# Kernel tuning notes

Measured on AMD Instinct MI355X. Metric: run time of the kernel, lower is better.

Reference implementation:

```python
import jax, jax.numpy as jnp
import numpy as np

KSIZE, SCALE, STRIDE, SOFTMAX_SCALE = 3, 3, 1, 10.0
ESCAPE_NAN = 1e-4
DN = ('NCHW', 'OIHW', 'NCHW')


def same_pad(x, k, stride):
    # torch same_padding: pad so out = ceil(in/stride)
    H, W = x.shape[-2], x.shape[-1]
    oh, ow = -(-H // stride), -(-W // stride)
    ph = max(0, (oh - 1) * stride + k - H)
    pw = max(0, (ow - 1) * stride + k - W)
    return jnp.pad(x, ((0, 0), (0, 0), (ph // 2, ph - ph // 2), (pw // 2, pw - pw // 2)))


def extract_patches(img, k, stride):
    # img [B,C,H,W] already padded -> [B, L, C, k, k], matching torch Unfold ordering (C slowest, kh, kw)
    B, C, H, W = img.shape
    oh, ow = (H - k) // stride + 1, (W - k) // stride + 1
    cols = [img[:, :, i:i + stride * oh:stride, j:j + stride * ow:stride]
            for i in range(k) for j in range(k)]
    p = jnp.stack(cols, axis=2)                      # [B, C, k*k, oh, ow]
    p = p.reshape(B, C, k, k, oh * ow)               # [B, C, k, k, L]
    return jnp.transpose(p, (0, 4, 1, 2, 3))         # [B, L, C, k, k]


def conv1x1_prelu(x, W, b, a):
    y = jnp.einsum('bchw,oc->bohw', x, W) + b[None, :, None, None]
    return jnp.where(y >= 0, y, a * y)


def bilinear_down(x, Ho, Wo):
    # F.interpolate(mode='bilinear', align_corners=False), no antialias
    H, W = x.shape[-2], x.shape[-1]
    def coords(o, s):
        src = (jnp.arange(o, dtype=jnp.float32) + 0.5) * (s / o) - 0.5
        src = jnp.clip(src, 0.0, s - 1.0)
        i0 = jnp.floor(src).astype(jnp.int32)
        i1 = jnp.minimum(i0 + 1, s - 1)
        return i0, i1, src - i0.astype(jnp.float32)
    y0, y1, wy = coords(Ho, H)
    x0, x1, wx = coords(Wo, W)
    r = x[:, :, y0, :] * (1.0 - wy)[:, None] + x[:, :, y1, :] * wy[:, None]
    return r[:, :, :, x0] * (1.0 - wx) + r[:, :, :, x1] * wx


def forward(x, Wa, ba, aa, Wm1, bm1, am1, Wm2, bm2, am2):
    B, C, H, W = x.shape
    kernel = SCALE * KSIZE  # 9
    embed_w = conv1x1_prelu(x, Wa, ba, aa)      # [B,C,H,W]
    match = conv1x1_prelu(x, Wm1, bm1, am1)     # [B,C/2,H,W]
    # large-scale patches used as conv_transpose kernels: [B, L, C, 9, 9]
    raw_w = extract_patches(same_pad(embed_w, kernel, STRIDE * SCALE), kernel, STRIDE * SCALE)
    Hr, Wr = H // SCALE, W // SCALE
    ref = conv1x1_prelu(bilinear_down(x, Hr, Wr), Wm2, bm2, am2)  # [B,C/2,Hr,Wr]
    # small-scale patches used as correlation kernels: [B, L, C/2, 3, 3]
    w = extract_patches(same_pad(ref, KSIZE, STRIDE), KSIZE, STRIDE)
    norm = jnp.sqrt(jnp.sum(w * w, axis=(2, 3, 4), keepdims=True))
    wn = w / jnp.maximum(norm, ESCAPE_NAN)
    xp = same_pad(match, KSIZE, 1)  # [B,C/2,H+2,W+2]

    def corr(xi, wi):  # xi [C/2,H+2,W+2], wi [L,C/2,3,3] -> [L,H,W]
        return jax.lax.conv_general_dilated(xi[None], wi, (1, 1), 'VALID', dimension_numbers=DN)[0]

    y = jax.vmap(corr)(xp, wn)                  # [B,L,H,W]
    y = jax.nn.softmax(y * SOFTMAX_SCALE, axis=1)

    pad = kernel - 1 - SCALE  # conv_transpose2d(stride=3, padding=3) equivalent padding = 5

    def tconv(yi, rwi):  # yi [L,H,W], rwi [L,C,9,9] -> [C,3H,3W]
        k = jnp.transpose(jnp.flip(rwi, (-2, -1)), (1, 0, 2, 3))  # [C,L,9,9]
        return jax.lax.conv_general_dilated(
            yi[None], k, (1, 1), [(pad, pad), (pad, pad)],
            lhs_dilation=(STRIDE * SCALE, STRIDE * SCALE), dimension_numbers=DN)[0]

    out = jax.vmap(tconv)(y, raw_w) / 6.0       # [B,C,3H,3W]
    return out


def setup_inputs() -> dict:
    key = jax.random.key(0)
    ks = jax.random.split(key, 8)
    B, C, H, W = 4, 64, 60, 60
    C2 = C // 2
    return {
        'x': jax.random.normal(ks[0], (B, C, H, W), jnp.float32),
        'Wa': jax.random.normal(ks[1], (C, C), jnp.float32) * 0.1,
        'ba': jax.random.normal(ks[2], (C,), jnp.float32) * 0.1,
        'aa': jnp.full((1,), 0.25, jnp.float32),
        'Wm1': jax.random.normal(ks[3], (C2, C), jnp.float32) * 0.1,
        'bm1': jax.random.normal(ks[4], (C2,), jnp.float32) * 0.1,
        'am1': jnp.full((1,), 0.25, jnp.float32),
        'Wm2': jax.random.normal(ks[5], (C2, C), jnp.float32) * 0.1,
        'bm2': jax.random.normal(ks[6], (C2,), jnp.float32) * 0.1,
        'am2': jnp.full((1,), 0.25, jnp.float32),
    }


def reference(x, Wa, ba, aa, Wm1, bm1, am1, Wm2, bm2, am2):
    return forward(x, Wa, ba, aa, Wm1, bm1, am1, Wm2, bm2, am2)
```

## Files before the change

### kernel.cpp

```cpp
#include <hip/hip_runtime.h>
#include <hip/hip_bf16.h>

typedef __hip_bfloat16 bf16_t;
using f32x4  = __attribute__((ext_vector_type(4))) float;
using bf16x8 = __attribute__((ext_vector_type(8))) short;

#define NB 4
#define NC 64
#define NC2 32
#define NH 60
#define NW 60
#define NPIX (NH*NW)
#define HP 66
#define MP 62
#define HR 20
#define RP 22
#define NL 400
#define OHW 180
#define KPAD 512

#define SZ_E   (NB*HP*HP*NC)
#define SZ_XP  (NB*NC2*MP*MP)
#define SZ_RP  (NB*NC2*RP*RP)
#define SZ_IN  (NB*NL)
#define SZ_Y   (NB*NPIX*NL)

__global__ __launch_bounds__(256) void k_conv(
    const float* __restrict__ x,
    const float* __restrict__ Wa,  const float* __restrict__ ba,  const float* __restrict__ aa,
    const float* __restrict__ Wm1, const float* __restrict__ bm1, const float* __restrict__ am1,
    const float* __restrict__ Wm2, const float* __restrict__ bm2, const float* __restrict__ am2,
    float* __restrict__ E_t, float* __restrict__ xp, float* __restrict__ refp) {
  int bid = blockIdx.x;
  int t = threadIdx.x;
  if (bid < 3600) {
    __shared__ float Ws[64*64];
    __shared__ float bs[64];
    __shared__ float al;
    int b = bid / 900, pblk = bid % 900;
    for (int i = t; i < 64*64; i += 256) {
      int co = i >> 6, c = i & 63;
      Ws[c*64 + co] = Wa[i];
    }
    if (t < 64) bs[t] = ba[t];
    if (t == 0) al = aa[0];
    __syncthreads();
    int lane = t & 63, wid = t >> 6;
    int pix = pblk*4 + wid;
    int ph = pix / NW, pw = pix % NW;
    const float* xb = x + b*NC*NPIX + pix;
    float acc = bs[lane];
    #pragma unroll 8
    for (int c = 0; c < 64; ++c)
      acc = fmaf(xb[c*NPIX], Ws[c*64 + lane], acc);
    acc = acc >= 0.f ? acc : al*acc;
    E_t[((b*HP + ph+3)*HP + (pw+3))*NC + lane] = acc;
  } else if (bid < 5400) {
    int idx = (bid - 3600)*256 + t;
    int pix = idx % NPIX; int tmp = idx / NPIX;
    int co = tmp % NC2; int b = tmp / NC2;
    float alpha = am1[0];
    const float* xb = x + b*NC*NPIX + pix;
    const float* wr = Wm1 + co*64;
    float acc = bm1[co];
    #pragma unroll 8
    for (int c = 0; c < 64; ++c)
      acc = fmaf(xb[c*NPIX], wr[c], acc);
    acc = acc >= 0.f ? acc : alpha*acc;
    int ph = pix / NW, pw = pix % NW;
    xp[((b*NC2 + co)*MP + ph+1)*MP + (pw+1)] = acc;
  } else {
    int idx = (bid - 5400)*256 + t;
    int pos = idx % (HR*HR); int tmp = idx / (HR*HR);
    int co = tmp % NC2; int b = tmp / NC2;
    int hr = pos / HR, wr_ = pos % HR;
    float alpha = am2[0];
    const float* xb = x + b*NC*NPIX + (3*hr+1)*NW + (3*wr_+1);
    const float* wrow = Wm2 + co*64;
    float acc = bm2[co];
    #pragma unroll 8
    for (int c = 0; c < 64; ++c)
      acc = fmaf(xb[c*NPIX], wrow[c], acc);
    acc = acc >= 0.f ? acc : alpha*acc;
    refp[((b*NC2 + co)*RP + hr+1)*RP + (wr_+1)] = acc;
  }
}

__global__ __launch_bounds__(64) void k_invn(
    const float* __restrict__ refp, float* __restrict__ invn) {
  int bl = blockIdx.x;
  int b = bl / NL, l = bl % NL;
  int lh = l / HR, lw = l % HR;
  int t = threadIdx.x;
  float ss = 0.f;
  for (int e = t; e < NC2*9; e += 64) {
    int c = e / 9, r = e % 9;
    int i = r / 3, j = r % 3;
    float v = refp[((b*NC2 + c)*RP + lh+i)*RP + (lw+j)];
    ss = fmaf(v, v, ss);
  }
  #pragma unroll
  for (int off = 32; off > 0; off >>= 1)
    ss += __shfl_xor(ss, off);
  if (t == 0) invn[bl] = 1.f / fmaxf(sqrtf(ss), 1e-4f);
}

__global__ __launch_bounds__(256) void k_swz(
    const float* __restrict__ xp, const float* __restrict__ refp,
    const float* __restrict__ invn, const float* __restrict__ E_t,
    bf16_t* __restrict__ Xp, bf16_t* __restrict__ Rf, bf16_t* __restrict__ Eb) {
  int bid = blockIdx.x;
  if (bid < 2025) {
    int tid = bid*256 + threadIdx.x;
    int slot = tid & 63; int rest = tid >> 6;
    int ks = rest % 9; int rest2 = rest / 9;
    int mblk = rest2 % 225; int b = rest2 / 225;
    int m = mblk*16 + (slot & 15);
    int h = m / NW, w = m % NW;
    int k0 = ks*32 + (slot >> 4)*8;
    const float* xb = xp + (size_t)b*NC2*MP*MP;
    union { bf16_t a[8]; bf16x8 v; } u;
    #pragma unroll
    for (int j = 0; j < 8; ++j) {
      int k = k0 + j;
      int c = k / 9, r = k % 9;
      int i = r / 3, j2 = r % 3;
      u.a[j] = __float2bfloat16(xb[(c*MP + h + i)*MP + w + j2]);
    }
    *(bf16x8*)(Xp + (size_t)tid*8) = u.v;
  } else if (bid < 2250) {
    int tid = (bid - 2025)*256 + threadIdx.x;
    int slot = tid & 63; int rest = tid >> 6;
    int ks = rest % 9; int rest2 = rest / 9;
    int nblk = rest2 % 25; int b = rest2 / 25;
    int l = nblk*16 + (slot & 15);
    int lh = l / HR, lw = l % HR;
    float sc = 10.f * invn[b*NL + l];
    int k0 = ks*32 + (slot >> 4)*8;
    const float* rb = refp + (size_t)b*NC2*RP*RP;
    union { bf16_t a[8]; bf16x8 v; } u;
    #pragma unroll
    for (int j = 0; j < 8; ++j) {
      int k = k0 + j;
      int c = k / 9, r = k % 9;
      int i = r / 3, j2 = r % 3;
      u.a[j] = __float2bfloat16(rb[(c*RP + lh + i)*RP + lw + j2] * sc);
    }
    *(bf16x8*)(Rf + (size_t)tid*8) = u.v;
  } else {
    int r2 = bid - 2250;
    int n = r2 % 576, b = r2 / 576;
    int c = n / 9, n9 = n % 9, rr = n9 / 3, s = n9 % 3;
    size_t nbase = ((size_t)(b*12 + n/48)*16);
    for (int k = threadIdx.x; k < KPAD; k += 256) {
      float v = 0.f;
      if (k < 484) {
        int u = k / 22, vv = k % 22;
        v = E_t[((size_t)((b*HP + 3*u + rr)*HP + 3*vv + s))*NC + c];
      }
      size_t idx = (((nbase + (k>>5))*3 + (n%48)/16)*64 + ((k>>3)&3)*16 + (n&15))*8 + (k&7);
      Eb[idx] = __float2bfloat16(v);
    }
  }
}

__global__ __launch_bounds__(64) void k_cgemm(
    const bf16x8* __restrict__ Xp, const bf16x8* __restrict__ Rf,
    bf16_t* __restrict__ y_bl) {
  int L = threadIdx.x;
  int nt = blockIdx.x, mt = blockIdx.y, b = blockIdx.z;
  const bf16x8* pa = Xp + ((size_t)(b*225 + mt*3)*9)*64 + L;
  const bf16x8* pb = Rf + ((size_t)(b*25 + nt*5)*9)*64 + L;
  f32x4 acc[3][5];
  #pragma unroll
  for (int i = 0; i < 3; ++i)
    #pragma unroll
    for (int j = 0; j < 5; ++j)
      acc[i][j] = {0.f, 0.f, 0.f, 0.f};
  bf16x8 af[3], bf[5], afn[3], bfn[5];
  #pragma unroll
  for (int i = 0; i < 3; ++i) af[i] = pa[i*576];
  #pragma unroll
  for (int j = 0; j < 5; ++j) bf[j] = pb[j*576];
  for (int ks = 0; ks < 9; ++ks) {
    if (ks < 8) {
      #pragma unroll
      for (int i = 0; i < 3; ++i) afn[i] = pa[i*576 + (ks+1)*64];
      #pragma unroll
      for (int j = 0; j < 5; ++j) bfn[j] = pb[j*576 + (ks+1)*64];
    }
    #pragma unroll
    for (int i = 0; i < 3; ++i)
      #pragma unroll
      for (int j = 0; j < 5; ++j)
        acc[i][j] = __builtin_amdgcn_mfma_f32_16x16x32_bf16(af[i], bf[j], acc[i][j], 0, 0, 0);
    #pragma unroll
    for (int i = 0; i < 3; ++i) af[i] = afn[i];
    #pragma unroll
    for (int j = 0; j < 5; ++j) bf[j] = bfn[j];
  }
  int quad = L >> 4, col = L & 15;
  #pragma unroll
  for (int mf = 0; mf < 3; ++mf) {
    #pragma unroll
    for (int r = 0; r < 4; ++r) {
      int m = mt*48 + mf*16 + quad*4 + r;
      bf16_t* row = y_bl + ((size_t)(b*NPIX + m))*NL + nt*80 + col;
      #pragma unroll
      for (int nf = 0; nf < 5; ++nf)
        row[nf*16] = __float2bfloat16(acc[mf][nf][r]);
    }
  }
}

__device__ __forceinline__ float lo_bf(unsigned int u) {
  return __uint_as_float(u << 16);
}
__device__ __forceinline__ float hi_bf(unsigned int u) {
  return __uint_as_float(u & 0xffff0000u);
}

__global__ __launch_bounds__(256) void k_saprime(
    const unsigned int* __restrict__ y_b32, bf16_t* __restrict__ Ap) {
  __shared__ uint4 raw[1728];
  unsigned short* ysp = (unsigned short*)raw;
  int t = threadIdx.x;
  int b = blockIdx.z;
  int h0base = blockIdx.y*2, w0base = blockIdx.x*4;
  for (int i = t; i < 1728; i += 256) raw[i] = uint4{0,0,0,0};
  __syncthreads();

  int wave = t >> 6, lane = t & 63;
  bool has4 = lane < 8;
  int hh = h0base - 1 + wave;
  bool hok = (unsigned)hh < NH;
  unsigned int vv[6][4];
  #pragma unroll
  for (int it = 0; it < 6; ++it) {
    int ww = w0base - 1 + it;
    if (hok && (unsigned)ww < NW) {
      const unsigned int* src = y_b32 + ((size_t)(b*NPIX + hh*NW + ww))*200;
      vv[it][0] = src[lane];
      vv[it][1] = src[lane+64];
      vv[it][2] = src[lane+128];
      vv[it][3] = has4 ? src[lane+192] : 0u;
    }
  }
  #pragma unroll
  for (int it = 0; it < 6; ++it) {
    int ww = w0base - 1 + it;
    if (!(hok && (unsigned)ww < NW)) continue;
    float f[8];
    #pragma unroll
    for (int k = 0; k < 3; ++k) {
      f[2*k]   = lo_bf(vv[it][k]);
      f[2*k+1] = hi_bf(vv[it][k]);
    }
    f[6] = has4 ? lo_bf(vv[it][3]) : -1e30f;
    f[7] = has4 ? hi_bf(vv[it][3]) : -1e30f;
    float m = -1e30f;
    #pragma unroll
    for (int k = 0; k < 8; ++k) m = fmaxf(m, f[k]);
    #pragma unroll
    for (int off = 32; off > 0; off >>= 1)
      m = fmaxf(m, __shfl_xor(m, off));
    float s = 0.f;
    #pragma unroll
    for (int k = 0; k < 8; ++k) {
      float e = expf(f[k] - m);
      f[k] = e;
      s += e;
    }
    #pragma unroll
    for (int off = 32; off > 0; off >>= 1)
      s += __shfl_xor(s, off);
    float r = 1.f / s;
    int pos = wave*6 + it;
    #pragma unroll
    for (int k = 0; k < 4; ++k) {
      if (k == 3 && !has4) break;
      int l2 = lane + 64*k;
      int lh = l2 / 10, lw = 2*l2 - 20*lh;
      union { bf16_t h[2]; unsigned int u; } pk;
      pk.h[0] = __float2bfloat16(f[2*k]   * r);
      pk.h[1] = __float2bfloat16(f[2*k+1] * r);
      *(unsigned int*)&ysp[pos*576 + (lh+2)*24 + (lw+2)] = pk.u;
    }
  }
  __syncthreads();

  int row = t >> 5;
  int klane = t & 31;
  int h0r = row >> 2, w0r = row & 3;
  int m = (h0base + h0r)*NW + (w0base + w0r);
  int pblk = m / 80, pf = (m % 80) >> 4, mrow = m & 15;
  size_t rowbase = ((size_t)(b*45 + pblk)*16);
  const unsigned short* basep = ysp + (h0r*6 + w0r)*576;
  for (int kk = 0; kk < 16; ++kk) {
    int k = kk*32 + klane;
    float acc = 0.f;
    if (k < 484) {
      int u = k / 22, v = k - 22*u;
      const unsigned short* q = basep + u*24 + v;
      #pragma unroll
      for (int dh = 0; dh < 3; ++dh) {
        #pragma unroll
        for (int dw = 0; dw < 3; ++dw) {
          unsigned short rbits = q[dh*3480 + dw*577];
          acc += __uint_as_float(((unsigned int)rbits) << 16);
        }
      }
    }
    size_t idx = (((rowbase + (k>>5))*5 + pf)*64 + ((k>>3)&3)*16 + mrow)*8 + (k&7);
    Ap[idx] = __float2bfloat16(acc);
  }
}

__global__ __launch_bounds__(64) void k_tgemm(
    const bf16x8* __restrict__ Eb, const bf16x8* __restrict__ Ap,
    float* __restrict__ out) {
  int L = threadIdx.x;
  int pb = blockIdx.x, rb = blockIdx.y, b = blockIdx.z;
  const bf16x8* pa = Eb + ((size_t)(b*12 + rb)*16)*3*64 + L;
  const bf16x8* pp = Ap + ((size_t)(b*45 + pb)*16)*5*64 + L;
  f32x4 acc[3][5];
  #pragma unroll
  for (int i = 0; i < 3; ++i)
    #pragma unroll
    for (int j = 0; j < 5; ++j)
      acc[i][j] = {0.f, 0.f, 0.f, 0.f};
  bf16x8 af[3], bf[5], afn[3], bfn[5];
  #pragma unroll
  for (int i = 0; i < 3; ++i) af[i] = pa[i*64];
  #pragma unroll
  for (int j = 0; j < 5; ++j) bf[j] = pp[j*64];
  for (int ks = 0; ks < 16; ++ks) {
    if (ks < 15) {
      const bf16x8* na = pa + (ks+1)*192;
      const bf16x8* nb = pp + (ks+1)*320;
      #pragma unroll
      for (int i = 0; i < 3; ++i) afn[i] = na[i*64];
      #pragma unroll
      for (int j = 0; j < 5; ++j) bfn[j] = nb[j*64];
    }
    #pragma unroll
    for (int i = 0; i < 3; ++i)
      #pragma unroll
      for (int j = 0; j < 5; ++j)
        acc[i][j] = __builtin_amdgcn_mfma_f32_16x16x32_bf16(af[i], bf[j], acc[i][j], 0, 0, 0);
    #pragma unroll
    for (int i = 0; i < 3; ++i) af[i] = afn[i];
    #pragma unroll
    for (int j = 0; j < 5; ++j) bf[j] = bfn[j];
  }
  int quad = L >> 4, col = L & 15;
  const float sc = 1.f/6.f;
  #pragma unroll
  for (int pf = 0; pf < 5; ++pf) {
    int m = pb*80 + pf*16 + col;
    int h0 = m / 60, w0 = m % 60;
    int posoff = b*(NC*OHW*OHW) + h0*540 + w0*3;
    #pragma unroll
    for (int rf = 0; rf < 3; ++rf) {
      #pragma unroll
      for (int r = 0; r < 4; ++r) {
        int n = rb*48 + rf*16 + quad*4 + r;
        int c = n / 9, n9 = n % 9;
        int rr = n9 / 3, s = n9 % 3;
        out[posoff + c*32400 + rr*180 + s] = acc[rf][pf][r] * sc;
      }
    }
  }
}

extern "C" void kernel_launch(void* const* d_in, const int* in_sizes, int n_in,
                              void* d_out, int out_size, void* d_ws, size_t ws_size,
                              hipStream_t stream) {
  (void)in_sizes; (void)n_in; (void)out_size; (void)ws_size;
  const float* x   = (const float*)d_in[0];
  const float* Wa  = (const float*)d_in[1];
  const float* ba  = (const float*)d_in[2];
  const float* aa  = (const float*)d_in[3];
  const float* Wm1 = (const float*)d_in[4];
  const float* bm1 = (const float*)d_in[5];
  const float* am1 = (const float*)d_in[6];
  const float* Wm2 = (const float*)d_in[7];
  const float* bm2 = (const float*)d_in[8];
  const float* am2 = (const float*)d_in[9];
  float* out = (float*)d_out;

  float* E_t  = (float*)d_ws;
  float* xp   = E_t + SZ_E;
  float* refp = xp + SZ_XP;
  float* invn = refp + SZ_RP;
  float* y_t  = invn + SZ_IN;
  bf16_t* y_bl = (bf16_t*)y_t;
  bf16_t* ApSwz = (bf16_t*)(y_t + SZ_Y);
  bf16_t* EbSwz = ApSwz + (size_t)NB*45*16*5*64*8;
  bf16_t* XpSwz = EbSwz + (size_t)NB*12*16*3*64*8;
  bf16_t* RfSwz = XpSwz + (size_t)NB*225*9*64*8;

  hipMemsetAsync(d_ws, 0, (size_t)(SZ_E + SZ_XP + SZ_RP)*sizeof(float), stream);

  k_conv<<<5600, 256, 0, stream>>>(x, Wa, ba, aa, Wm1, bm1, am1, Wm2, bm2, am2,
                                   E_t, xp, refp);
  k_invn<<<NB*NL, 64, 0, stream>>>(refp, invn);
  k_swz<<<4554, 256, 0, stream>>>(xp, refp, invn, E_t, XpSwz, RfSwz, EbSwz);
  k_cgemm<<<dim3(5, 75, NB), 64, 0, stream>>>((const bf16x8*)XpSwz, (const bf16x8*)RfSwz, y_bl);
  k_saprime<<<dim3(15, 30, NB), 256, 0, stream>>>((const unsigned int*)y_bl, ApSwz);
  k_tgemm<<<dim3(45, 12, NB), 64, 0, stream>>>((const bf16x8*)EbSwz, (const bf16x8*)ApSwz, out);
}
```

Before: 201.6 us.

## Fuse patch-norm kernel into swizzle and enlarge softmax tiles

Removes the separate k_invn launch by computing each reference patch's inverse L2 norm inside the Rf swizzle blocks, with the scale shared through LDS. k_saprime now covers a 4x4 output tile with 512 threads instead of 2x4 with 256, which cuts redundant halo softmax recomputation. It also switches expf to __expf. The trade-offs are more LDS per block, a less register-heavy but serial per-wave loop, and slightly lower exp precision.

```diff
diff --git a/kernel.cpp b/kernel.cpp
--- a/kernel.cpp
+++ b/kernel.cpp
@@ -86,32 +86,15 @@
   }
 }
 
-__global__ __launch_bounds__(64) void k_invn(
-    const float* __restrict__ refp, float* __restrict__ invn) {
-  int bl = blockIdx.x;
-  int b = bl / NL, l = bl % NL;
-  int lh = l / HR, lw = l % HR;
-  int t = threadIdx.x;
-  float ss = 0.f;
-  for (int e = t; e < NC2*9; e += 64) {
-    int c = e / 9, r = e % 9;
-    int i = r / 3, j = r % 3;
-    float v = refp[((b*NC2 + c)*RP + lh+i)*RP + (lw+j)];
-    ss = fmaf(v, v, ss);
-  }
-  #pragma unroll
-  for (int off = 32; off > 0; off >>= 1)
-    ss += __shfl_xor(ss, off);
-  if (t == 0) invn[bl] = 1.f / fmaxf(sqrtf(ss), 1e-4f);
-}
-
 __global__ __launch_bounds__(256) void k_swz(
     const float* __restrict__ xp, const float* __restrict__ refp,
-    const float* __restrict__ invn, const float* __restrict__ E_t,
+    const float* __restrict__ E_t,
     bf16_t* __restrict__ Xp, bf16_t* __restrict__ Rf, bf16_t* __restrict__ Eb) {
+  __shared__ float scl[16];
   int bid = blockIdx.x;
+  int t = threadIdx.x;
   if (bid < 2025) {
-    int tid = bid*256 + threadIdx.x;
+    int tid = bid*256 + t;
     int slot = tid & 63; int rest = tid >> 6;
     int ks = rest % 9; int rest2 = rest / 9;
     int mblk = rest2 % 225; int b = rest2 / 225;
@@ -128,31 +111,49 @@
       u.a[j] = __float2bfloat16(xb[(c*MP + h + i)*MP + w + j2]);
     }
     *(bf16x8*)(Xp + (size_t)tid*8) = u.v;
-  } else if (bid < 2250) {
-    int tid = (bid - 2025)*256 + threadIdx.x;
-    int slot = tid & 63; int rest = tid >> 6;
-    int ks = rest % 9; int rest2 = rest / 9;
-    int nblk = rest2 % 25; int b = rest2 / 25;
-    int l = nblk*16 + (slot & 15);
+  } else if (bid < 2125) {
+    int r2 = bid - 2025;
+    int nblk = r2 % 25, b = r2 / 25;
+    int ll = t >> 4, sub = t & 15;
+    int l = nblk*16 + ll;
     int lh = l / HR, lw = l % HR;
-    float sc = 10.f * invn[b*NL + l];
-    int k0 = ks*32 + (slot >> 4)*8;
     const float* rb = refp + (size_t)b*NC2*RP*RP;
-    union { bf16_t a[8]; bf16x8 v; } u;
-    #pragma unroll
-    for (int j = 0; j < 8; ++j) {
-      int k = k0 + j;
-      int c = k / 9, r = k % 9;
-      int i = r / 3, j2 = r % 3;
-      u.a[j] = __float2bfloat16(rb[(c*RP + lh + i)*RP + lw + j2] * sc);
-    }
-    *(bf16x8*)(Rf + (size_t)tid*8) = u.v;
+    float ss = 0.f;
+    #pragma unroll
+    for (int e0 = 0; e0 < 18; ++e0) {
+      int e = sub*18 + e0;
+      int c = e / 9, r = e % 9;
+      int i = r / 3, j = r % 3;
+      float v = rb[(c*RP + lh + i)*RP + lw + j];
+      ss = fmaf(v, v, ss);
+    }
+    #pragma unroll
+    for (int off = 1; off < 16; off <<= 1)
+      ss += __shfl_xor(ss, off);
+    if (sub == 0) scl[ll] = 10.f / fmaxf(sqrtf(ss), 1e-4f);
+    __syncthreads();
+    for (int sidx = t; sidx < 576; sidx += 256) {
+      int ks = sidx >> 6, slot = sidx & 63;
+      int l2 = nblk*16 + (slot & 15);
+      int lh2 = l2 / HR, lw2 = l2 % HR;
+      float sc = scl[slot & 15];
+      int k0 = ks*32 + (slot >> 4)*8;
+      union { bf16_t a[8]; bf16x8 v; } u;
+      #pragma unroll
+      for (int j = 0; j < 8; ++j) {
+        int k = k0 + j;
+        int c = k / 9, r = k % 9;
+        int i = r / 3, j2 = r % 3;
+        u.a[j] = __float2bfloat16(rb[(c*RP + lh2 + i)*RP + lw2 + j2] * sc);
+      }
+      *(bf16x8*)(Rf + ((size_t)(b*25 + nblk)*576 + sidx)*8) = u.v;
+    }
   } else {
-    int r2 = bid - 2250;
+    int r2 = bid - 2125;
     int n = r2 % 576, b = r2 / 576;
     int c = n / 9, n9 = n % 9, rr = n9 / 3, s = n9 % 3;
     size_t nbase = ((size_t)(b*12 + n/48)*16);
-    for (int k = threadIdx.x; k < KPAD; k += 256) {
+    for (int k = t; k < KPAD; k += 256) {
       float v = 0.f;
       if (k < 484) {
         int u = k / 22, vv = k % 22;
@@ -220,44 +221,33 @@
   return __uint_as_float(u & 0xffff0000u);
 }
 
-__global__ __launch_bounds__(256) void k_saprime(
+__global__ __launch_bounds__(512) void k_saprime(
     const unsigned int* __restrict__ y_b32, bf16_t* __restrict__ Ap) {
-  __shared__ uint4 raw[1728];
+  __shared__ uint4 raw[2592];
   unsigned short* ysp = (unsigned short*)raw;
   int t = threadIdx.x;
   int b = blockIdx.z;
-  int h0base = blockIdx.y*2, w0base = blockIdx.x*4;
-  for (int i = t; i < 1728; i += 256) raw[i] = uint4{0,0,0,0};
+  int h0base = blockIdx.y*4, w0base = blockIdx.x*4;
+  for (int i = t; i < 2592; i += 512) raw[i] = uint4{0,0,0,0};
   __syncthreads();
 
   int wave = t >> 6, lane = t & 63;
   bool has4 = lane < 8;
-  int hh = h0base - 1 + wave;
-  bool hok = (unsigned)hh < NH;
-  unsigned int vv[6][4];
-  #pragma unroll
-  for (int it = 0; it < 6; ++it) {
-    int ww = w0base - 1 + it;
-    if (hok && (unsigned)ww < NW) {
-      const unsigned int* src = y_b32 + ((size_t)(b*NPIX + hh*NW + ww))*200;
-      vv[it][0] = src[lane];
-      vv[it][1] = src[lane+64];
-      vv[it][2] = src[lane+128];
-      vv[it][3] = has4 ? src[lane+192] : 0u;
-    }
-  }
-  #pragma unroll
-  for (int it = 0; it < 6; ++it) {
-    int ww = w0base - 1 + it;
-    if (!(hok && (unsigned)ww < NW)) continue;
+  for (int pos = wave; pos < 36; pos += 8) {
+    int i = pos / 6, jj = pos % 6;
+    int hh = h0base - 1 + i, ww = w0base - 1 + jj;
+    if (!((unsigned)hh < NH && (unsigned)ww < NW)) continue;
+    const unsigned int* src = y_b32 + ((size_t)(b*NPIX + hh*NW + ww))*200;
+    unsigned int v0 = src[lane];
+    unsigned int v1 = src[lane+64];
+    unsigned int v2 = src[lane+128];
+    unsigned int v3 = has4 ? src[lane+192] : 0u;
     float f[8];
-    #pragma unroll
-    for (int k = 0; k < 3; ++k) {
-      f[2*k]   = lo_bf(vv[it][k]);
-      f[2*k+1] = hi_bf(vv[it][k]);
-    }
-    f[6] = has4 ? lo_bf(vv[it][3]) : -1e30f;
-    f[7] = has4 ? hi_bf(vv[it][3]) : -1e30f;
+    f[0] = lo_bf(v0); f[1] = hi_bf(v0);
+    f[2] = lo_bf(v1); f[3] = hi_bf(v1);
+    f[4] = lo_bf(v2); f[5] = hi_bf(v2);
+    f[6] = has4 ? lo_bf(v3) : -1e30f;
+    f[7] = has4 ? hi_bf(v3) : -1e30f;
     float m = -1e30f;
     #pragma unroll
     for (int k = 0; k < 8; ++k) m = fmaxf(m, f[k]);
@@ -267,7 +257,7 @@
     float s = 0.f;
     #pragma unroll
     for (int k = 0; k < 8; ++k) {
-      float e = expf(f[k] - m);
+      float e = __expf(f[k] - m);
       f[k] = e;
       s += e;
     }
@@ -275,7 +265,6 @@
     for (int off = 32; off > 0; off >>= 1)
       s += __shfl_xor(s, off);
     float r = 1.f / s;
-    int pos = wave*6 + it;
     #pragma unroll
     for (int k = 0; k < 4; ++k) {
       if (k == 3 && !has4) break;
@@ -392,8 +381,7 @@
   float* E_t  = (float*)d_ws;
   float* xp   = E_t + SZ_E;
   float* refp = xp + SZ_XP;
-  float* invn = refp + SZ_RP;
-  float* y_t  = invn + SZ_IN;
+  float* y_t  = refp + SZ_RP + SZ_IN;
   bf16_t* y_bl = (bf16_t*)y_t;
   bf16_t* ApSwz = (bf16_t*)(y_t + SZ_Y);
   bf16_t* EbSwz = ApSwz + (size_t)NB*45*16*5*64*8;
@@ -404,9 +392,8 @@
 
   k_conv<<<5600, 256, 0, stream>>>(x, Wa, ba, aa, Wm1, bm1, am1, Wm2, bm2, am2,
                                    E_t, xp, refp);
-  k_invn<<<NB*NL, 64, 0, stream>>>(refp, invn);
-  k_swz<<<4554, 256, 0, stream>>>(xp, refp, invn, E_t, XpSwz, RfSwz, EbSwz);
+  k_swz<<<4429, 256, 0, stream>>>(xp, refp, E_t, XpSwz, RfSwz, EbSwz);
   k_cgemm<<<dim3(5, 75, NB), 64, 0, stream>>>((const bf16x8*)XpSwz, (const bf16x8*)RfSwz, y_bl);
-  k_saprime<<<dim3(15, 30, NB), 256, 0, stream>>>((const unsigned int*)y_bl, ApSwz);
+  k_saprime<<<dim3(15, 15, NB), 512, 0, stream>>>((const unsigned int*)y_bl, ApSwz);
   k_tgemm<<<dim3(45, 12, NB), 64, 0, stream>>>((const bf16x8*)EbSwz, (const bf16x8*)ApSwz, out);
 }
```

After: 189.8 us. 5.9% less time.
